# Performance work log

Measured on AMD Instinct MI355X. Metric: run time of the kernel, lower is better.

The kernel has to match this reference:

```python
import jax, jax.numpy as jnp
import numpy as np

DIM, HEAD, SR = 512, 8, 2
LN_EPS = 1e-5


def _layernorm(x, g, b):
    mu = jnp.mean(x, axis=-1, keepdims=True)
    var = jnp.mean((x - mu) ** 2, axis=-1, keepdims=True)
    return (x - mu) * jax.lax.rsqrt(var + LN_EPS) * g + b


def setup_inputs() -> dict:
    key = jax.random.key(0)
    ks = jax.random.split(key, 16)
    B, N, C = 8, 4096, DIM
    s = 1.0 / np.sqrt(C)
    inp = {
        "x": jax.random.normal(ks[0], (B, N, C), jnp.float32),
        "context": jax.random.normal(ks[1], (B, N, C), jnp.float32),
        # Linear weights in torch layout [out, in]
        "Wq": jax.random.normal(ks[2], (C, C), jnp.float32) * s,
        "bq": jnp.zeros((C,), jnp.float32),
        "Wk": jax.random.normal(ks[3], (C, C), jnp.float32) * s,
        "bk": jnp.zeros((C,), jnp.float32),
        "Wv": jax.random.normal(ks[4], (C, C), jnp.float32) * s,
        "bv": jnp.zeros((C,), jnp.float32),
        "Wp": jax.random.normal(ks[5], (C, C), jnp.float32) * s,
        "bp": jnp.zeros((C,), jnp.float32),
        # spatial-reduction convs, OIHW, kernel=stride=SR
        "Wsrk": jax.random.normal(ks[6], (C, C, SR, SR), jnp.float32) * s / SR,
        "bsrk": jnp.zeros((C,), jnp.float32),
        "Wsrv": jax.random.normal(ks[7], (C, C, SR, SR), jnp.float32) * s / SR,
        "bsrv": jnp.zeros((C,), jnp.float32),
        "gk": jnp.ones((C,), jnp.float32),
        "bek": jnp.zeros((C,), jnp.float32),
        "gv": jnp.ones((C,), jnp.float32),
        "bev": jnp.zeros((C,), jnp.float32),
        "H": 64,
        "W": 64,
    }
    return inp


def reference(x, context, Wq, bq, Wk, bk, Wv, bv, Wp, bp,
              Wsrk, bsrk, Wsrv, bsrv, gk, bek, gv, bev, H, W):
    B, N, C = x.shape
    h, d = HEAD, C // HEAD
    scale = d ** (-0.5)

    # spatial reduction on context (sr_ratio > 1 branch)
    ctx = jnp.transpose(context, (0, 2, 1)).reshape(B, C, H, W)  # [B,C,H,W]
    dn = (("NCHW", "OIHW", "NCHW"))

    def sr(kernel, bias):
        y = jax.lax.conv_general_dilated(ctx, kernel, (SR, SR), "VALID",
                                         dimension_numbers=dn)
        y = y + bias[None, :, None, None]
        return jnp.transpose(y.reshape(B, C, -1), (0, 2, 1))  # [B,M,C]

    ctx_k = _layernorm(sr(Wsrk, bsrk), gk, bek)
    ctx_v = _layernorm(sr(Wsrv, bsrv), gv, bev)

    q = (x @ Wq.T + bq).reshape(B, N, h, d)          # [B,N,h,d]
    k = (ctx_k @ Wk.T + bk).reshape(B, -1, h, d)     # [B,M,h,d]
    v = (ctx_v @ Wv.T + bv).reshape(B, -1, h, d)     # [B,M,h,d]

    attn = jnp.einsum("bnhd,bmhd->bhnm", q, k) * scale
    attn = jax.nn.softmax(attn, axis=-1)
    out = jnp.einsum("bhnm,bmhd->bnhd", attn, v).reshape(B, N, C)
    return out @ Wp.T + bp
```

## Files before the change

### kernel.cpp

```cpp
#include <hip/hip_runtime.h>
#include <hip/hip_bf16.h>

typedef float f32x4 __attribute__((ext_vector_type(4)));
typedef short bf16x8 __attribute__((ext_vector_type(8)));
typedef unsigned short ushort_t;

__device__ __forceinline__ ushort_t f2bf(float f) {
    union { float f; unsigned u; } v; v.f = f;
    unsigned r = v.u + 0x7fffu + ((v.u >> 16) & 1u);
    return (ushort_t)(r >> 16);
}
__device__ __forceinline__ float bf2f(ushort_t h) {
    union { unsigned u; float f; } v; v.u = ((unsigned)h) << 16;
    return v.f;
}

__device__ __forceinline__ void async16(ushort_t* lds, const ushort_t* g) {
    __builtin_amdgcn_global_load_lds(
        (const __attribute__((address_space(1))) unsigned int*)g,
        (__attribute__((address_space(3))) unsigned int*)lds, 16, 0, 0);
}

__global__ __launch_bounds__(256) void cast_bf16_kernel(const float* __restrict__ src,
                                                        ushort_t* __restrict__ dst, long n) {
    long i = ((long)blockIdx.x * 256 + threadIdx.x) * 8;
    if (i >= n) return;
    float4 a = *(const float4*)(src + i);
    float4 b = *(const float4*)(src + i + 4);
    ushort_t o[8];
    o[0]=f2bf(a.x); o[1]=f2bf(a.y); o[2]=f2bf(a.z); o[3]=f2bf(a.w);
    o[4]=f2bf(b.x); o[5]=f2bf(b.y); o[6]=f2bf(b.z); o[7]=f2bf(b.w);
    *(bf16x8*)(dst + i) = *(bf16x8*)o;
}

__global__ __launch_bounds__(256) void cast_w4_kernel(const float* __restrict__ s0,
                                                      const float* __restrict__ s1,
                                                      const float* __restrict__ s2,
                                                      const float* __restrict__ s3,
                                                      ushort_t* __restrict__ dst) {
    long idx = (long)blockIdx.x * 256 + threadIdx.x;
    int sel = (int)(idx >> 15);
    const float* s = sel == 0 ? s0 : sel == 1 ? s1 : sel == 2 ? s2 : s3;
    long off = (idx & 32767) * 8;
    float4 a = *(const float4*)(s + off);
    float4 b = *(const float4*)(s + off + 4);
    ushort_t o[8];
    o[0]=f2bf(a.x); o[1]=f2bf(a.y); o[2]=f2bf(a.z); o[3]=f2bf(a.w);
    o[4]=f2bf(b.x); o[5]=f2bf(b.y); o[6]=f2bf(b.z); o[7]=f2bf(b.w);
    *(bf16x8*)(dst + (long)sel * 262144 + off) = *(bf16x8*)o;
}

__global__ __launch_bounds__(256) void pack_wsr2_kernel(const float* __restrict__ w0,
                                                        const float* __restrict__ w1,
                                                        ushort_t* __restrict__ out) {
    int idx = blockIdx.x * 256 + threadIdx.x;
    int sel = idx >> 20;
    const float* w = sel ? w1 : w0;
    int li = idx & 1048575;
    int c = li >> 11, k = li & 2047;
    int tap = k >> 9, ci = k & 511;
    out[idx] = f2bf(w[c * 2048 + ci * 4 + tap]);
}

struct GemmJob {
    const ushort_t* A;
    const ushort_t* Bw;
    const float* bias;
    void* C;
    int omode;
};

template<bool GATHER>
__global__ __launch_bounds__(256) void gemm_bt(GemmJob j0, GemmJob j1,
                                               int M, int N, int K) {
    __shared__ __align__(16) ushort_t As[128][64];
    __shared__ __align__(16) ushort_t Bs[128][64];
    const GemmJob j = blockIdx.z == 0 ? j0 : j1;
    const int tid  = threadIdx.x;
    const int row0 = blockIdx.y * 128, col0 = blockIdx.x * 128;
    const int wave = tid >> 6, lane = tid & 63;
    const int rw = wave >> 1, cw = wave & 1;
    const int l15 = lane & 15, l4 = lane >> 4;
    const int srow = wave * 8 + (lane >> 3);
    const int sc8  = (lane & 7) * 8;

    f32x4 acc[4][4] = {};

    for (int k0 = 0; k0 < K; k0 += 64) {
        __syncthreads();
#pragma unroll
        for (int p = 0; p < 4; ++p) {
            int r = p * 32 + srow;
            const ushort_t* ga;
            if (GATHER) {
                int gr = row0 + r;
                int b = gr >> 10, m = gr & 1023;
                int mh = m >> 5, mw = m & 31;
                int tap = k0 >> 9;
                int kh = tap >> 1, kw = tap & 1;
                ga = j.A + ((long)(b * 4096 + (2 * mh + kh) * 64 + (2 * mw + kw))) * 512
                         + (k0 & 511) + sc8;
            } else {
                ga = j.A + (long)(row0 + r) * K + k0 + sc8;
            }
            async16(&As[p * 32 + wave * 8][0], ga);
            async16(&Bs[p * 32 + wave * 8][0],
                    j.Bw + (long)(col0 + r) * K + k0 + sc8);
        }
        __syncthreads();
#pragma unroll
        for (int ks = 0; ks < 2; ++ks) {
            bf16x8 af[4], bfr[4];
#pragma unroll
            for (int i = 0; i < 4; ++i)
                af[i] = *(const bf16x8*)&As[rw * 64 + i * 16 + l15][ks * 32 + l4 * 8];
#pragma unroll
            for (int jj = 0; jj < 4; ++jj)
                bfr[jj] = *(const bf16x8*)&Bs[cw * 64 + jj * 16 + l15][ks * 32 + l4 * 8];
#pragma unroll
            for (int i = 0; i < 4; ++i)
#pragma unroll
                for (int jj = 0; jj < 4; ++jj)
                    acc[i][jj] = __builtin_amdgcn_mfma_f32_16x16x32_bf16(af[i], bfr[jj],
                                                                         acc[i][jj], 0, 0, 0);
        }
    }
#pragma unroll
    for (int i = 0; i < 4; ++i) {
#pragma unroll
        for (int jj = 0; jj < 4; ++jj) {
            int col = col0 + cw * 64 + jj * 16 + l15;
            float bv = j.bias[col];
#pragma unroll
            for (int r = 0; r < 4; ++r) {
                int row = row0 + rw * 64 + i * 16 + l4 * 4 + r;
                float v = acc[i][jj][r] + bv;
                if (j.omode == 0) {
                    ((ushort_t*)j.C)[(long)row * N + col] = f2bf(v);
                } else if (j.omode == 1) {
                    ((float*)j.C)[(long)row * N + col] = v;
                } else {
                    int b = row >> 10, m = row & 1023;
                    int hh = col >> 6, dd = col & 63;
                    ((ushort_t*)j.C)[(((long)(b * 8 + hh) * 64 + dd) << 10) + m] = f2bf(v);
                }
            }
        }
    }
}

__global__ __launch_bounds__(256) void ln_kernel(ushort_t* __restrict__ data,
                                                 const float* __restrict__ g0,
                                                 const float* __restrict__ be0,
                                                 const float* __restrict__ g1,
                                                 const float* __restrict__ be1) {
    int wave = threadIdx.x >> 6, lane = threadIdx.x & 63;
    long row = (long)blockIdx.x * 4 + wave;
    const float* g  = row < 8192 ? g0 : g1;
    const float* be = row < 8192 ? be0 : be1;
    ushort_t* p = data + row * 512 + lane * 8;
    bf16x8 raw = *(bf16x8*)p;
    ushort_t* rp = (ushort_t*)&raw;
    float v[8], s = 0.f, s2 = 0.f;
#pragma unroll
    for (int j = 0; j < 8; ++j) { v[j] = bf2f(rp[j]); s += v[j]; s2 += v[j] * v[j]; }
#pragma unroll
    for (int d = 1; d < 64; d <<= 1) { s += __shfl_xor(s, d); s2 += __shfl_xor(s2, d); }
    float mu  = s * (1.f / 512.f);
    float var = s2 * (1.f / 512.f) - mu * mu;
    float rs  = rsqrtf(var + 1e-5f);
    ushort_t o[8];
#pragma unroll
    for (int j = 0; j < 8; ++j) {
        int c = lane * 8 + j;
        o[j] = f2bf((v[j] - mu) * rs * g[c] + be[c]);
    }
    *(bf16x8*)p = *(bf16x8*)o;
}

__global__ __launch_bounds__(256, 3) void attn_kernel(const ushort_t* __restrict__ q,
                                                      const ushort_t* __restrict__ k,
                                                      const ushort_t* __restrict__ vt,
                                                      ushort_t* __restrict__ o) {
    __shared__ __align__(16) ushort_t Ks[128][72];
    __shared__ __align__(16) ushort_t Vs[64][136];

    const int tid = threadIdx.x;
    const int wave = tid >> 6, lane = tid & 63;
    const int l15 = lane & 15, l4 = lane >> 4;
    const int n0 = blockIdx.x * 128;
    const int hh = blockIdx.y;
    const int b  = blockIdx.z;

    bf16x8 bq[2][2];
#pragma unroll
    for (int nb = 0; nb < 2; ++nb)
#pragma unroll
        for (int ks = 0; ks < 2; ++ks)
            bq[nb][ks] = *(const bf16x8*)(
                q + (long)(b * 4096 + n0 + wave * 32 + nb * 16 + l15) * 512
                  + hh * 64 + ks * 32 + l4 * 8);

    f32x4 oacc[2][4] = {};
    f32x4 lacc[2] = {};
    union { bf16x8 v8; unsigned u[4]; } ones;
    ones.u[0] = ones.u[1] = ones.u[2] = ones.u[3] = 0x3F803F80u;
    const float EC = 0.18033688011112042f;

    for (int c = 0; c < 8; ++c) {
        const int m0 = c * 128;
        __syncthreads();
#pragma unroll
        for (int p = 0; p < 4; ++p) {
            int qi = p * 256 + tid;
            int r = qi >> 3, c8 = (qi & 7) * 8;
            bf16x8 v = *(const bf16x8*)(k + (((long)(b * 1024 + m0 + r) * 8 + hh) << 6) + c8);
            *(bf16x8*)&Ks[r][c8] = v;
        }
#pragma unroll
        for (int p = 0; p < 4; ++p) {
            int qi = p * 256 + tid;
            int dd = qi >> 4, c8 = (qi & 15) * 8;
            bf16x8 v = *(const bf16x8*)(vt + (((long)(b * 8 + hh) * 64 + dd) << 10) + m0 + c8);
            *(bf16x8*)&Vs[dd][c8] = v;
        }
        __syncthreads();

        f32x4 s[2][8] = {};
        __builtin_amdgcn_s_setprio(1);
#pragma unroll
        for (int ks = 0; ks < 2; ++ks) {
#pragma unroll
            for (int i = 0; i < 8; ++i) {
                bf16x8 ak = *(const bf16x8*)&Ks[i * 16 + l15][ks * 32 + l4 * 8];
                s[0][i] = __builtin_amdgcn_mfma_f32_16x16x32_bf16(ak, bq[0][ks], s[0][i], 0, 0, 0);
                s[1][i] = __builtin_amdgcn_mfma_f32_16x16x32_bf16(ak, bq[1][ks], s[1][i], 0, 0, 0);
            }
        }
        __builtin_amdgcn_s_setprio(0);

        unsigned pk[2][8][2];
#pragma unroll
        for (int nb = 0; nb < 2; ++nb)
#pragma unroll
            for (int i = 0; i < 8; ++i) {
                float e0 = __builtin_amdgcn_exp2f(s[nb][i][0] * EC);
                float e1 = __builtin_amdgcn_exp2f(s[nb][i][1] * EC);
                float e2 = __builtin_amdgcn_exp2f(s[nb][i][2] * EC);
                float e3 = __builtin_amdgcn_exp2f(s[nb][i][3] * EC);
                asm("v_cvt_pk_bf16_f32 %0, %1, %2" : "=v"(pk[nb][i][0]) : "v"(e0), "v"(e1));
                asm("v_cvt_pk_bf16_f32 %0, %1, %2" : "=v"(pk[nb][i][1]) : "v"(e2), "v"(e3));
            }

        __builtin_amdgcn_s_setprio(1);
#pragma unroll
        for (int mb = 0; mb < 4; ++mb) {
            union { bf16x8 v8; unsigned long long h[2]; } bfr[4];
#pragma unroll
            for (int db = 0; db < 4; ++db) {
                bfr[db].h[0] = *(const unsigned long long*)&Vs[db * 16 + l15][mb * 32 + l4 * 4];
                bfr[db].h[1] = *(const unsigned long long*)&Vs[db * 16 + l15][mb * 32 + 16 + l4 * 4];
            }
#pragma unroll
            for (int nb = 0; nb < 2; ++nb) {
                union { bf16x8 v8; unsigned u32v[4]; } af;
                af.u32v[0] = pk[nb][2 * mb][0];
                af.u32v[1] = pk[nb][2 * mb][1];
                af.u32v[2] = pk[nb][2 * mb + 1][0];
                af.u32v[3] = pk[nb][2 * mb + 1][1];
                lacc[nb] = __builtin_amdgcn_mfma_f32_16x16x32_bf16(af.v8, ones.v8,
                                                                   lacc[nb], 0, 0, 0);
#pragma unroll
                for (int db = 0; db < 4; ++db)
                    oacc[nb][db] = __builtin_amdgcn_mfma_f32_16x16x32_bf16(af.v8, bfr[db].v8,
                                                                           oacc[nb][db], 0, 0, 0);
            }
        }
        __builtin_amdgcn_s_setprio(0);
    }

#pragma unroll
    for (int nb = 0; nb < 2; ++nb)
#pragma unroll
        for (int r = 0; r < 4; ++r) {
            float inv = 1.f / lacc[nb][r];
            int n = wave * 32 + nb * 16 + l4 * 4 + r;
#pragma unroll
            for (int db = 0; db < 4; ++db) {
                int dd = db * 16 + l15;
                o[((long)(b * 4096 + n0 + n)) * 512 + hh * 64 + dd] = f2bf(oacc[nb][db][r] * inv);
            }
        }
}

extern "C" void kernel_launch(void* const* d_in, const int* in_sizes, int n_in,
                              void* d_out, int out_size, void* d_ws, size_t ws_size,
                              hipStream_t stream) {
    const float* x    = (const float*)d_in[0];
    const float* ctx  = (const float*)d_in[1];
    const float* Wq   = (const float*)d_in[2];
    const float* bq   = (const float*)d_in[3];
    const float* Wk   = (const float*)d_in[4];
    const float* bk   = (const float*)d_in[5];
    const float* Wv   = (const float*)d_in[6];
    const float* bv   = (const float*)d_in[7];
    const float* Wp   = (const float*)d_in[8];
    const float* bp   = (const float*)d_in[9];
    const float* Wsrk = (const float*)d_in[10];
    const float* bsrk = (const float*)d_in[11];
    const float* Wsrv = (const float*)d_in[12];
    const float* bsrv = (const float*)d_in[13];
    const float* gk   = (const float*)d_in[14];
    const float* bek  = (const float*)d_in[15];
    const float* gv   = (const float*)d_in[16];
    const float* bev  = (const float*)d_in[17];

    ushort_t* x_bf    = (ushort_t*)d_ws;
    ushort_t* ctx_bf  = x_bf    + 16777216;
    ushort_t* q_bf    = ctx_bf  + 16777216;
    ushort_t* at_bf   = q_bf    + 16777216;
    ushort_t* k_bf    = at_bf   + 16777216;
    ushort_t* vt_bf   = k_bf    + 4194304;
    ushort_t* convk   = vt_bf   + 4194304;
    ushort_t* convv   = convk   + 4194304;
    ushort_t* wq_bf   = convv   + 4194304;
    ushort_t* wk_bf   = wq_bf   + 262144;
    ushort_t* wv_bf   = wk_bf   + 262144;
    ushort_t* wp_bf   = wv_bf   + 262144;
    ushort_t* wsrk_p  = wp_bf   + 262144;
    ushort_t* wsrv_p  = wsrk_p  + 1048576;

    cast_bf16_kernel<<<8192, 256, 0, stream>>>(x,   x_bf,   16777216);
    cast_bf16_kernel<<<8192, 256, 0, stream>>>(ctx, ctx_bf, 16777216);
    cast_w4_kernel<<<512, 256, 0, stream>>>(Wq, Wk, Wv, Wp, wq_bf);
    pack_wsr2_kernel<<<8192, 256, 0, stream>>>(Wsrk, Wsrv, wsrk_p);

    GemmJob jck = { ctx_bf, wsrk_p, bsrk, convk, 0 };
    GemmJob jcv = { ctx_bf, wsrv_p, bsrv, convv, 0 };
    gemm_bt<true><<<dim3(4, 64, 2), 256, 0, stream>>>(jck, jcv, 8192, 512, 2048);

    ln_kernel<<<4096, 256, 0, stream>>>(convk, gk, bek, gv, bev);

    GemmJob jq  = { x_bf,  wq_bf, bq, q_bf, 0 };
    gemm_bt<false><<<dim3(4, 256, 1), 256, 0, stream>>>(jq, jq, 32768, 512, 512);
    GemmJob jk  = { convk, wk_bf, bk, k_bf, 0 };
    GemmJob jv  = { convv, wv_bf, bv, vt_bf, 2 };
    gemm_bt<false><<<dim3(4, 64, 2), 256, 0, stream>>>(jk, jv, 8192, 512, 512);

    attn_kernel<<<dim3(32, 8, 8), 256, 0, stream>>>(q_bf, k_bf, vt_bf, at_bf);

    GemmJob jo  = { at_bf, wp_bf, bp, d_out, 1 };
    gemm_bt<false><<<dim3(4, 256, 1), 256, 0, stream>>>(jo, jo, 32768, 512, 512);
}
```

Baseline: 478.4 us.

## Merge conv and Q GEMMs into one multi-job launch, vectorize weight packing

Replaces the templated two-job GEMM with a runtime-dispatched kernel that takes three jobs over a flat block index. This lets the two spatial-reduction conv GEMMs and the Q projection run in a single launch, filling the GPU better and removing one kernel launch. The weight pack kernel now reads float4 per thread and writes the four taps separately, so it needs fewer threads and does coalesced reads. The cost is a runtime branch on the gather mode in the inner loop, which may add register pressure or change code generation for every GEMM.

```diff
diff --git a/kernel.cpp b/kernel.cpp
--- a/kernel.cpp
+++ b/kernel.cpp
@@ -54,12 +54,16 @@
                                                         const float* __restrict__ w1,
                                                         ushort_t* __restrict__ out) {
     int idx = blockIdx.x * 256 + threadIdx.x;
-    int sel = idx >> 20;
+    int sel = idx >> 18;
     const float* w = sel ? w1 : w0;
-    int li = idx & 1048575;
-    int c = li >> 11, k = li & 2047;
-    int tap = k >> 9, ci = k & 511;
-    out[idx] = f2bf(w[c * 2048 + ci * 4 + tap]);
+    int li = idx & 262143;
+    int c = li >> 9, ci = li & 511;
+    float4 t = *(const float4*)(w + c * 2048 + ci * 4);
+    ushort_t* ob = out + sel * 1048576 + c * 2048 + ci;
+    ob[0]    = f2bf(t.x);
+    ob[512]  = f2bf(t.y);
+    ob[1024] = f2bf(t.z);
+    ob[1536] = f2bf(t.w);
 }
 
 struct GemmJob {
@@ -68,21 +72,30 @@
     const float* bias;
     void* C;
     int omode;
+    int M;
+    int K;
+    int gather;
 };
 
-template<bool GATHER>
-__global__ __launch_bounds__(256) void gemm_bt(GemmJob j0, GemmJob j1,
-                                               int M, int N, int K) {
+__global__ __launch_bounds__(256) void gemm_multi(GemmJob j0, GemmJob j1, GemmJob j2,
+                                                  int nb0, int nb1) {
     __shared__ __align__(16) ushort_t As[128][64];
     __shared__ __align__(16) ushort_t Bs[128][64];
-    const GemmJob j = blockIdx.z == 0 ? j0 : j1;
+    const int bid = blockIdx.x;
+    GemmJob j;
+    int local;
+    if (bid < nb0)            { j = j0; local = bid; }
+    else if (bid < nb0 + nb1) { j = j1; local = bid - nb0; }
+    else                      { j = j2; local = bid - nb0 - nb1; }
+
     const int tid  = threadIdx.x;
-    const int row0 = blockIdx.y * 128, col0 = blockIdx.x * 128;
+    const int row0 = (local >> 2) * 128, col0 = (local & 3) * 128;
     const int wave = tid >> 6, lane = tid & 63;
     const int rw = wave >> 1, cw = wave & 1;
     const int l15 = lane & 15, l4 = lane >> 4;
     const int srow = wave * 8 + (lane >> 3);
     const int sc8  = (lane & 7) * 8;
+    const int K = j.K;
 
     f32x4 acc[4][4] = {};
 
@@ -92,7 +105,7 @@
         for (int p = 0; p < 4; ++p) {
             int r = p * 32 + srow;
             const ushort_t* ga;
-            if (GATHER) {
+            if (j.gather) {
                 int gr = row0 + r;
                 int b = gr >> 10, m = gr & 1023;
                 int mh = m >> 5, mw = m & 31;
@@ -136,9 +149,9 @@
                 int row = row0 + rw * 64 + i * 16 + l4 * 4 + r;
                 float v = acc[i][jj][r] + bv;
                 if (j.omode == 0) {
-                    ((ushort_t*)j.C)[(long)row * N + col] = f2bf(v);
+                    ((ushort_t*)j.C)[(long)row * 512 + col] = f2bf(v);
                 } else if (j.omode == 1) {
-                    ((float*)j.C)[(long)row * N + col] = v;
+                    ((float*)j.C)[(long)row * 512 + col] = v;
                 } else {
                     int b = row >> 10, m = row & 1023;
                     int hh = col >> 6, dd = col & 63;
@@ -333,22 +346,21 @@
     cast_bf16_kernel<<<8192, 256, 0, stream>>>(x,   x_bf,   16777216);
     cast_bf16_kernel<<<8192, 256, 0, stream>>>(ctx, ctx_bf, 16777216);
     cast_w4_kernel<<<512, 256, 0, stream>>>(Wq, Wk, Wv, Wp, wq_bf);
-    pack_wsr2_kernel<<<8192, 256, 0, stream>>>(Wsrk, Wsrv, wsrk_p);
-
-    GemmJob jck = { ctx_bf, wsrk_p, bsrk, convk, 0 };
-    GemmJob jcv = { ctx_bf, wsrv_p, bsrv, convv, 0 };
-    gemm_bt<true><<<dim3(4, 64, 2), 256, 0, stream>>>(jck, jcv, 8192, 512, 2048);
+    pack_wsr2_kernel<<<2048, 256, 0, stream>>>(Wsrk, Wsrv, wsrk_p);
+
+    GemmJob jck = { ctx_bf, wsrk_p, bsrk, convk, 0, 8192,  2048, 1 };
+    GemmJob jcv = { ctx_bf, wsrv_p, bsrv, convv, 0, 8192,  2048, 1 };
+    GemmJob jq  = { x_bf,  wq_bf,  bq,   q_bf,  0, 32768, 512,  0 };
+    gemm_multi<<<1536, 256, 0, stream>>>(jck, jcv, jq, 256, 256);
 
     ln_kernel<<<4096, 256, 0, stream>>>(convk, gk, bek, gv, bev);
 
-    GemmJob jq  = { x_bf,  wq_bf, bq, q_bf, 0 };
-    gemm_bt<false><<<dim3(4, 256, 1), 256, 0, stream>>>(jq, jq, 32768, 512, 512);
-    GemmJob jk  = { convk, wk_bf, bk, k_bf, 0 };
-    GemmJob jv  = { convv, wv_bf, bv, vt_bf, 2 };
-    gemm_bt<false><<<dim3(4, 64, 2), 256, 0, stream>>>(jk, jv, 8192, 512, 512);
+    GemmJob jk  = { convk, wk_bf, bk, k_bf,  0, 8192, 512, 0 };
+    GemmJob jv  = { convv, wv_bf, bv, vt_bf, 2, 8192, 512, 0 };
+    gemm_multi<<<512, 256, 0, stream>>>(jk, jv, jv, 256, 256);
 
     attn_kernel<<<dim3(32, 8, 8), 256, 0, stream>>>(q_bf, k_bf, vt_bf, at_bf);
 
-    GemmJob jo  = { at_bf, wp_bf, bp, d_out, 1 };
-    gemm_bt<false><<<dim3(4, 256, 1), 256, 0, stream>>>(jo, jo, 32768, 512, 512);
-}
+    GemmJob jo  = { at_bf, wp_bf, bp, d_out, 1, 32768, 512, 0 };
+    gemm_multi<<<1024, 256, 0, stream>>>(jo, jo, jo, 1024, 0);
+}
```

After: 454.2 us. -5.1%, faster.
